# Optimization experiments

Measured on AMD Instinct MI355X. Metric: run time of the kernel, lower is better.

Reference implementation:

```python
import jax, jax.numpy as jnp
import numpy as np

B, N, A = 4096, 16, 8          # envs, num_agents, num_actions
D_IN, H1, DP, DZ = 128, 64, 64, 64  # obs dim, gnn hidden, obs_proc dim, gat fc dim


def _init(k, shape):
    return jax.random.normal(k, shape, jnp.float32) / np.sqrt(shape[0]).astype(np.float32)


def setup_inputs() -> dict:
    key = jax.random.key(0)
    ks = jax.random.split(key, 8)
    return {
        "obs": jax.random.normal(ks[0], (B * N, D_IN), jnp.float32),
        "policies": jax.random.uniform(ks[1], (B * N, A), dtype=jnp.float32),
        "actions": jax.random.uniform(ks[2], (B * N, A), dtype=jnp.float32),
        "W1": _init(ks[3], (D_IN, H1)), "b1": jnp.zeros((H1,), jnp.float32),
        "W2": _init(ks[4], (H1, DP)), "b2": jnp.zeros((DP,), jnp.float32),
        "Wfc": _init(ks[5], (DP, DZ)),
        "Wattn": _init(ks[6], (2 * DZ, 1)),
        "Wv": _init(ks[7], (DP + A, 1)), "bv": jnp.zeros((1,), jnp.float32),
    }


def reference(obs, policies, actions, W1, b1, W2, b2, Wfc, Wattn, Wv, bv):
    obs = obs.reshape(B, N, D_IN)
    # --- CriticInputPreprocess: two mean-aggregation GNN layers on a complete
    # graph with self-loops -> every node sees the per-env mean.
    agg1 = jnp.mean(obs, axis=1)                      # [B, D_IN]
    h = jax.nn.relu(agg1 @ W1 + b1)                   # [B, H1] (identical across nodes)
    obs_proc1 = h @ W2 + b2                           # mean of identical features is itself
    obs_proc = jnp.broadcast_to(obs_proc1[:, None, :], (B, N, DP))  # [B, N, DP]
    # --- GATLayer edge attention: e_{d<-s} = leaky_relu(attn([z_s, z_d]))
    z_ = obs_proc @ Wfc                               # [B, N, DZ]
    a_src = (z_ @ Wattn[:DZ]).squeeze(-1)             # [B, N]
    a_dst = (z_ @ Wattn[DZ:]).squeeze(-1)             # [B, N]
    e = jax.nn.leaky_relu(a_src[:, None, :] + a_dst[:, :, None])    # [B, dst, src]
    w = jax.nn.sigmoid(e)                             # [B, N, N]
    pi = policies.reshape(B, N, A)
    act = actions.reshape(B, N, A)
    # mailbox mix per (dst d, src k): z = w*act_k + (1-w)*pi_k
    z = w[..., None] * act[:, None, :, :] + (1.0 - w[..., None]) * pi[:, None, :, :]  # [B,d,k,A]
    # place_policies/place_zs + mean over src axis collapses to:
    # y[b,d,j] = (pi[b,j] + sum_{k!=j} z[b,d,k]) / N
    y = (jnp.sum(z, axis=2, keepdims=True) - z + pi[:, None, :, :]) / N               # [B,d,j,A]
    obs_rep = jnp.broadcast_to(obs_proc[:, None, :, :], (B, N, N, DP))                # obs_proc[b, j]
    obs_final = jnp.concatenate([obs_rep, y], axis=-1).reshape(B * N, N, DP + A)
    x = obs_final @ Wv + bv                           # [B*N, N, 1]
    return x, w.reshape(B * N, N, 1)
```

## Files before the change

kernel.cpp:

```cpp
#include <hip/hip_runtime.h>

#define BB   4096
#define NN   16
#define AA   8
#define DIN  128
#define H1C  64
#define DPC  64
#define DZC  64

#define GENV 8
#define WENV 4
#define NTHR 128

__global__ __launch_bounds__(NTHR, 1)
void critic_kernel(const float* __restrict__ obs,
                   const float* __restrict__ policies,
                   const float* __restrict__ actions,
                   const float* __restrict__ W1,
                   const float* __restrict__ b1,
                   const float* __restrict__ W2,
                   const float* __restrict__ b2,
                   const float* __restrict__ Wfc,
                   const float* __restrict__ Wattn,
                   const float* __restrict__ Wv,
                   const float* __restrict__ bv,
                   float* __restrict__ out_x,
                   float* __restrict__ out_w)
{
    __shared__ float sW1[DIN * H1C];
    __shared__ float sW2[H1C * DPC];
    __shared__ float sWfc[DPC * DZC];
    __shared__ float sAgg[GENV][DIN];
    __shared__ float sH[GENV][H1C];
    __shared__ float sP[GENV][DPC];
    __shared__ float sDv[GENV][16];

    const int tid = threadIdx.x;
    const int l   = tid & 63;
    const int wv  = tid >> 6;
    const int le0 = wv * WENV;
    const int e0  = blockIdx.x * GENV + le0;

    const float b1v = b1[l];
    const float b2v = b2[l];
    const float wa0 = Wattn[l];
    const float wa1 = Wattn[DZC + l];
    const float wvv = Wv[l];
    const float va  = Wv[64 + (l & 7)];
    const float bvv = bv[0];

    {
        const float4* g1 = reinterpret_cast<const float4*>(W1);
        float4*       s1 = reinterpret_cast<float4*>(sW1);
        #pragma unroll
        for (int i = 0; i < (DIN * H1C / 4) / NTHR; ++i)
            s1[i * NTHR + tid] = g1[i * NTHR + tid];
        const float4* g2 = reinterpret_cast<const float4*>(W2);
        float4*       s2 = reinterpret_cast<float4*>(sW2);
        #pragma unroll
        for (int i = 0; i < (H1C * DPC / 4) / NTHR; ++i)
            s2[i * NTHR + tid] = g2[i * NTHR + tid];
        const float4* g3 = reinterpret_cast<const float4*>(Wfc);
        float4*       s3 = reinterpret_cast<float4*>(sWfc);
        #pragma unroll
        for (int i = 0; i < (DPC * DZC / 4) / NTHR; ++i)
            s3[i * NTHR + tid] = g3[i * NTHR + tid];
    }

    #pragma unroll
    for (int ee = 0; ee < WENV; ++ee) {
        const float4* o4 = reinterpret_cast<const float4*>(obs + (size_t)(e0 + ee) * NN * DIN);
        float4 a = make_float4(0.f, 0.f, 0.f, 0.f);
        #pragma unroll
        for (int t = 0; t < 8; ++t) {
            const float4 v = o4[t * 64 + l];
            a.x += v.x; a.y += v.y; a.z += v.z; a.w += v.w;
        }
        a.x += __shfl_xor(a.x, 32);
        a.y += __shfl_xor(a.y, 32);
        a.z += __shfl_xor(a.z, 32);
        a.w += __shfl_xor(a.w, 32);
        if (l < 32) {
            const float inv = 1.0f / 16.0f;
            reinterpret_cast<float4*>(sAgg[le0 + ee])[l] =
                make_float4(a.x * inv, a.y * inv, a.z * inv, a.w * inv);
        }
    }

    float pv0[WENV], pv1[WENV], av0[WENV], av1[WENV];
    #pragma unroll
    for (int ee = 0; ee < WENV; ++ee) {
        const float* Pb = policies + (size_t)(e0 + ee) * (NN * AA);
        const float* Ab = actions  + (size_t)(e0 + ee) * (NN * AA);
        pv0[ee] = Pb[l]; pv1[ee] = Pb[64 + l];
        av0[ee] = Ab[l]; av1[ee] = Ab[64 + l];
    }

    __syncthreads();

    float acc0 = b1v, acc1 = b1v, acc2 = b1v, acc3 = b1v;
    #pragma unroll 8
    for (int d4 = 0; d4 < DIN / 4; ++d4) {
        const float w0  = sW1[(4 * d4 + 0) * H1C + l];
        const float w1_ = sW1[(4 * d4 + 1) * H1C + l];
        const float w2_ = sW1[(4 * d4 + 2) * H1C + l];
        const float w3_ = sW1[(4 * d4 + 3) * H1C + l];
        const float4 a0 = *reinterpret_cast<const float4*>(&sAgg[le0 + 0][4 * d4]);
        const float4 a1 = *reinterpret_cast<const float4*>(&sAgg[le0 + 1][4 * d4]);
        const float4 a2 = *reinterpret_cast<const float4*>(&sAgg[le0 + 2][4 * d4]);
        const float4 a3 = *reinterpret_cast<const float4*>(&sAgg[le0 + 3][4 * d4]);
        acc0 = fmaf(a0.x, w0, acc0); acc0 = fmaf(a0.y, w1_, acc0);
        acc0 = fmaf(a0.z, w2_, acc0); acc0 = fmaf(a0.w, w3_, acc0);
        acc1 = fmaf(a1.x, w0, acc1); acc1 = fmaf(a1.y, w1_, acc1);
        acc1 = fmaf(a1.z, w2_, acc1); acc1 = fmaf(a1.w, w3_, acc1);
        acc2 = fmaf(a2.x, w0, acc2); acc2 = fmaf(a2.y, w1_, acc2);
        acc2 = fmaf(a2.z, w2_, acc2); acc2 = fmaf(a2.w, w3_, acc2);
        acc3 = fmaf(a3.x, w0, acc3); acc3 = fmaf(a3.y, w1_, acc3);
        acc3 = fmaf(a3.z, w2_, acc3); acc3 = fmaf(a3.w, w3_, acc3);
    }
    sH[le0 + 0][l] = fmaxf(acc0, 0.0f);
    sH[le0 + 1][l] = fmaxf(acc1, 0.0f);
    sH[le0 + 2][l] = fmaxf(acc2, 0.0f);
    sH[le0 + 3][l] = fmaxf(acc3, 0.0f);

    __syncthreads();

    acc0 = b2v; acc1 = b2v; acc2 = b2v; acc3 = b2v;
    #pragma unroll
    for (int k4 = 0; k4 < H1C / 4; ++k4) {
        const float w0  = sW2[(4 * k4 + 0) * DPC + l];
        const float w1_ = sW2[(4 * k4 + 1) * DPC + l];
        const float w2_ = sW2[(4 * k4 + 2) * DPC + l];
        const float w3_ = sW2[(4 * k4 + 3) * DPC + l];
        const float4 a0 = *reinterpret_cast<const float4*>(&sH[le0 + 0][4 * k4]);
        const float4 a1 = *reinterpret_cast<const float4*>(&sH[le0 + 1][4 * k4]);
        const float4 a2 = *reinterpret_cast<const float4*>(&sH[le0 + 2][4 * k4]);
        const float4 a3 = *reinterpret_cast<const float4*>(&sH[le0 + 3][4 * k4]);
        acc0 = fmaf(a0.x, w0, acc0); acc0 = fmaf(a0.y, w1_, acc0);
        acc0 = fmaf(a0.z, w2_, acc0); acc0 = fmaf(a0.w, w3_, acc0);
        acc1 = fmaf(a1.x, w0, acc1); acc1 = fmaf(a1.y, w1_, acc1);
        acc1 = fmaf(a1.z, w2_, acc1); acc1 = fmaf(a1.w, w3_, acc1);
        acc2 = fmaf(a2.x, w0, acc2); acc2 = fmaf(a2.y, w1_, acc2);
        acc2 = fmaf(a2.z, w2_, acc2); acc2 = fmaf(a2.w, w3_, acc2);
        acc3 = fmaf(a3.x, w0, acc3); acc3 = fmaf(a3.y, w1_, acc3);
        acc3 = fmaf(a3.z, w2_, acc3); acc3 = fmaf(a3.w, w3_, acc3);
    }
    sP[le0 + 0][l] = acc0;
    sP[le0 + 1][l] = acc1;
    sP[le0 + 2][l] = acc2;
    sP[le0 + 3][l] = acc3;

    __syncthreads();

    float z0 = 0.f, z1 = 0.f, z2 = 0.f, z3 = 0.f;
    #pragma unroll
    for (int k4 = 0; k4 < DPC / 4; ++k4) {
        const float w0  = sWfc[(4 * k4 + 0) * DZC + l];
        const float w1_ = sWfc[(4 * k4 + 1) * DZC + l];
        const float w2_ = sWfc[(4 * k4 + 2) * DZC + l];
        const float w3_ = sWfc[(4 * k4 + 3) * DZC + l];
        const float4 a0 = *reinterpret_cast<const float4*>(&sP[le0 + 0][4 * k4]);
        const float4 a1 = *reinterpret_cast<const float4*>(&sP[le0 + 1][4 * k4]);
        const float4 a2 = *reinterpret_cast<const float4*>(&sP[le0 + 2][4 * k4]);
        const float4 a3 = *reinterpret_cast<const float4*>(&sP[le0 + 3][4 * k4]);
        z0 = fmaf(a0.x, w0, z0); z0 = fmaf(a0.y, w1_, z0);
        z0 = fmaf(a0.z, w2_, z0); z0 = fmaf(a0.w, w3_, z0);
        z1 = fmaf(a1.x, w0, z1); z1 = fmaf(a1.y, w1_, z1);
        z1 = fmaf(a1.z, w2_, z1); z1 = fmaf(a1.w, w3_, z1);
        z2 = fmaf(a2.x, w0, z2); z2 = fmaf(a2.y, w1_, z2);
        z2 = fmaf(a2.z, w2_, z2); z2 = fmaf(a2.w, w3_, z2);
        z3 = fmaf(a3.x, w0, z3); z3 = fmaf(a3.y, w1_, z3);
        z3 = fmaf(a3.z, w2_, z3); z3 = fmaf(a3.w, w3_, z3);
    }
    const float zz[WENV] = {z0, z1, z2, z3};

    float wgt[WENV], cc[WENV], Svv[WENV];
    #pragma unroll
    for (int ee = 0; ee < WENV; ++ee) {
        const int le = le0 + ee;
        float t0 = zz[ee] * (wa0 + wa1);
        float t1 = sP[le][l] * wvv;
        #pragma unroll
        for (int m = 32; m >= 1; m >>= 1) {
            t0 += __shfl_xor(t0, m);
            t1 += __shfl_xor(t1, m);
        }
        const float eV = (t0 > 0.0f) ? t0 : 0.01f * t0;
        wgt[ee] = 1.0f / (1.0f + expf(-eV));
        cc[ee]  = t1 + bvv;

        float q0 = (pv0[ee] - av0[ee]) * va;
        float q1 = (pv1[ee] - av1[ee]) * va;
        float fq = q0 + q1;
        float fp = (pv0[ee] + pv1[ee]) * va;
        #pragma unroll
        for (int m = 1; m <= 4; m <<= 1) {
            q0 += __shfl_xor(q0, m);
            q1 += __shfl_xor(q1, m);
        }
        #pragma unroll
        for (int m = 32; m >= 1; m >>= 1) {
            fq += __shfl_xor(fq, m);
            fp += __shfl_xor(fp, m);
        }
        Svv[ee] = fp - wgt[ee] * fq;

        if ((l & 7) == 0) {
            sDv[le][l >> 3]       = q0;
            sDv[le][8 + (l >> 3)] = q1;
        }
    }

    __syncthreads();

    const float invN = 1.0f / 16.0f;
    const int j0 = (4 * l) & 15;
    #pragma unroll
    for (int ee = 0; ee < WENV; ++ee) {
        const int le = le0 + ee;
        float4 xo, wo;
        xo.x = fmaf(wgt[ee], sDv[le][j0 + 0], Svv[ee]) * invN + cc[ee];
        xo.y = fmaf(wgt[ee], sDv[le][j0 + 1], Svv[ee]) * invN + cc[ee];
        xo.z = fmaf(wgt[ee], sDv[le][j0 + 2], Svv[ee]) * invN + cc[ee];
        xo.w = fmaf(wgt[ee], sDv[le][j0 + 3], Svv[ee]) * invN + cc[ee];
        wo.x = wo.y = wo.z = wo.w = wgt[ee];

        const size_t base = (size_t)(e0 + ee) * (NN * NN) + 4 * l;
        *reinterpret_cast<float4*>(out_x + base) = xo;
        *reinterpret_cast<float4*>(out_w + base) = wo;
    }
}

extern "C" void kernel_launch(void* const* d_in, const int* in_sizes, int n_in,
                              void* d_out, int out_size, void* d_ws, size_t ws_size,
                              hipStream_t stream) {
    const float* obs      = (const float*)d_in[0];
    const float* policies = (const float*)d_in[1];
    const float* actions  = (const float*)d_in[2];
    const float* W1       = (const float*)d_in[3];
    const float* b1       = (const float*)d_in[4];
    const float* W2       = (const float*)d_in[5];
    const float* b2       = (const float*)d_in[6];
    const float* Wfc      = (const float*)d_in[7];
    const float* Wattn    = (const float*)d_in[8];
    const float* Wv       = (const float*)d_in[9];
    const float* bv       = (const float*)d_in[10];

    float* out_x = (float*)d_out;
    float* out_w = out_x + (size_t)BB * NN * NN;

    critic_kernel<<<BB / GENV, NTHR, 0, stream>>>(obs, policies, actions,
                                                  W1, b1, W2, b2, Wfc, Wattn, Wv, bv,
                                                  out_x, out_w);
}
```

Measured before the change: 21.00 us.

## Fold W2, Wfc and attention/value weights into per-block vectors

Uses associativity to collapse the W2 and Wfc matmuls into two 64-vectors: u = Wfc·(wa_src+wa_dst) and v1 = W2·u, v2 = W2·Wv, plus bias scalars. After the W1 layer, each env then needs only dot products instead of two more 64x64 matmuls and their shared-memory staging and barriers. It also changes block shape to 256 threads with 2 envs per wave and allows two blocks per CU. The trade-off is that every block recomputes the folded vectors from global W2/Wfc, and the rounding order changes slightly.

```diff
diff --git a/kernel.cpp b/kernel.cpp
--- a/kernel.cpp
+++ b/kernel.cpp
@@ -9,10 +9,10 @@
 #define DZC  64
 
 #define GENV 8
-#define WENV 4
-#define NTHR 128
-
-__global__ __launch_bounds__(NTHR, 1)
+#define WENV 2
+#define NTHR 256
+
+__global__ __launch_bounds__(NTHR, 2)
 void critic_kernel(const float* __restrict__ obs,
                    const float* __restrict__ policies,
                    const float* __restrict__ actions,
@@ -28,11 +28,10 @@
                    float* __restrict__ out_w)
 {
     __shared__ float sW1[DIN * H1C];
-    __shared__ float sW2[H1C * DPC];
-    __shared__ float sWfc[DPC * DZC];
     __shared__ float sAgg[GENV][DIN];
-    __shared__ float sH[GENV][H1C];
-    __shared__ float sP[GENV][DPC];
+    __shared__ float sWsum[DZC];
+    __shared__ float sWv64[DPC];
+    __shared__ float sU[DPC];
     __shared__ float sDv[GENV][16];
 
     const int tid = threadIdx.x;
@@ -55,16 +54,6 @@
         #pragma unroll
         for (int i = 0; i < (DIN * H1C / 4) / NTHR; ++i)
             s1[i * NTHR + tid] = g1[i * NTHR + tid];
-        const float4* g2 = reinterpret_cast<const float4*>(W2);
-        float4*       s2 = reinterpret_cast<float4*>(sW2);
-        #pragma unroll
-        for (int i = 0; i < (H1C * DPC / 4) / NTHR; ++i)
-            s2[i * NTHR + tid] = g2[i * NTHR + tid];
-        const float4* g3 = reinterpret_cast<const float4*>(Wfc);
-        float4*       s3 = reinterpret_cast<float4*>(sWfc);
-        #pragma unroll
-        for (int i = 0; i < (DPC * DZC / 4) / NTHR; ++i)
-            s3[i * NTHR + tid] = g3[i * NTHR + tid];
     }
 
     #pragma unroll
@@ -96,9 +85,54 @@
         av0[ee] = Ab[l]; av1[ee] = Ab[64 + l];
     }
 
+    if (tid < 64) {
+        sWsum[l] = wa0 + wa1;
+        sWv64[l] = wvv;
+    }
+
     __syncthreads();
 
-    float acc0 = b1v, acc1 = b1v, acc2 = b1v, acc3 = b1v;
+    float u = 0.0f;
+    {
+        const float4* WfcR = reinterpret_cast<const float4*>(Wfc + (size_t)l * DZC);
+        const float4* ws4  = reinterpret_cast<const float4*>(sWsum);
+        #pragma unroll
+        for (int j4 = 0; j4 < DZC / 4; ++j4) {
+            const float4 w = WfcR[j4];
+            const float4 s = ws4[j4];
+            u = fmaf(w.x, s.x, u); u = fmaf(w.y, s.y, u);
+            u = fmaf(w.z, s.z, u); u = fmaf(w.w, s.w, u);
+        }
+    }
+    sU[l] = u;
+
+    __syncthreads();
+
+    float v1 = 0.0f, v2 = 0.0f;
+    {
+        const float4* W2R = reinterpret_cast<const float4*>(W2 + (size_t)l * DPC);
+        const float4* su4 = reinterpret_cast<const float4*>(sU);
+        const float4* sv4 = reinterpret_cast<const float4*>(sWv64);
+        #pragma unroll
+        for (int j4 = 0; j4 < DPC / 4; ++j4) {
+            const float4 w = W2R[j4];
+            const float4 a = su4[j4];
+            const float4 b = sv4[j4];
+            v1 = fmaf(w.x, a.x, v1); v1 = fmaf(w.y, a.y, v1);
+            v1 = fmaf(w.z, a.z, v1); v1 = fmaf(w.w, a.w, v1);
+            v2 = fmaf(w.x, b.x, v2); v2 = fmaf(w.y, b.y, v2);
+            v2 = fmaf(w.z, b.z, v2); v2 = fmaf(w.w, b.w, v2);
+        }
+    }
+    float tb2u = b2v * u;
+    float tb2w = b2v * wvv;
+    #pragma unroll
+    for (int m = 32; m >= 1; m >>= 1) {
+        tb2u += __shfl_xor(tb2u, m);
+        tb2w += __shfl_xor(tb2w, m);
+    }
+
+    float acc0 = b1v, acc1 = b1v;
     #pragma unroll 8
     for (int d4 = 0; d4 < DIN / 4; ++d4) {
         const float w0  = sW1[(4 * d4 + 0) * H1C + l];
@@ -107,87 +141,28 @@
         const float w3_ = sW1[(4 * d4 + 3) * H1C + l];
         const float4 a0 = *reinterpret_cast<const float4*>(&sAgg[le0 + 0][4 * d4]);
         const float4 a1 = *reinterpret_cast<const float4*>(&sAgg[le0 + 1][4 * d4]);
-        const float4 a2 = *reinterpret_cast<const float4*>(&sAgg[le0 + 2][4 * d4]);
-        const float4 a3 = *reinterpret_cast<const float4*>(&sAgg[le0 + 3][4 * d4]);
         acc0 = fmaf(a0.x, w0, acc0); acc0 = fmaf(a0.y, w1_, acc0);
         acc0 = fmaf(a0.z, w2_, acc0); acc0 = fmaf(a0.w, w3_, acc0);
         acc1 = fmaf(a1.x, w0, acc1); acc1 = fmaf(a1.y, w1_, acc1);
         acc1 = fmaf(a1.z, w2_, acc1); acc1 = fmaf(a1.w, w3_, acc1);
-        acc2 = fmaf(a2.x, w0, acc2); acc2 = fmaf(a2.y, w1_, acc2);
-        acc2 = fmaf(a2.z, w2_, acc2); acc2 = fmaf(a2.w, w3_, acc2);
-        acc3 = fmaf(a3.x, w0, acc3); acc3 = fmaf(a3.y, w1_, acc3);
-        acc3 = fmaf(a3.z, w2_, acc3); acc3 = fmaf(a3.w, w3_, acc3);
-    }
-    sH[le0 + 0][l] = fmaxf(acc0, 0.0f);
-    sH[le0 + 1][l] = fmaxf(acc1, 0.0f);
-    sH[le0 + 2][l] = fmaxf(acc2, 0.0f);
-    sH[le0 + 3][l] = fmaxf(acc3, 0.0f);
-
-    __syncthreads();
-
-    acc0 = b2v; acc1 = b2v; acc2 = b2v; acc3 = b2v;
-    #pragma unroll
-    for (int k4 = 0; k4 < H1C / 4; ++k4) {
-        const float w0  = sW2[(4 * k4 + 0) * DPC + l];
-        const float w1_ = sW2[(4 * k4 + 1) * DPC + l];
-        const float w2_ = sW2[(4 * k4 + 2) * DPC + l];
-        const float w3_ = sW2[(4 * k4 + 3) * DPC + l];
-        const float4 a0 = *reinterpret_cast<const float4*>(&sH[le0 + 0][4 * k4]);
-        const float4 a1 = *reinterpret_cast<const float4*>(&sH[le0 + 1][4 * k4]);
-        const float4 a2 = *reinterpret_cast<const float4*>(&sH[le0 + 2][4 * k4]);
-        const float4 a3 = *reinterpret_cast<const float4*>(&sH[le0 + 3][4 * k4]);
-        acc0 = fmaf(a0.x, w0, acc0); acc0 = fmaf(a0.y, w1_, acc0);
-        acc0 = fmaf(a0.z, w2_, acc0); acc0 = fmaf(a0.w, w3_, acc0);
-        acc1 = fmaf(a1.x, w0, acc1); acc1 = fmaf(a1.y, w1_, acc1);
-        acc1 = fmaf(a1.z, w2_, acc1); acc1 = fmaf(a1.w, w3_, acc1);
-        acc2 = fmaf(a2.x, w0, acc2); acc2 = fmaf(a2.y, w1_, acc2);
-        acc2 = fmaf(a2.z, w2_, acc2); acc2 = fmaf(a2.w, w3_, acc2);
-        acc3 = fmaf(a3.x, w0, acc3); acc3 = fmaf(a3.y, w1_, acc3);
-        acc3 = fmaf(a3.z, w2_, acc3); acc3 = fmaf(a3.w, w3_, acc3);
-    }
-    sP[le0 + 0][l] = acc0;
-    sP[le0 + 1][l] = acc1;
-    sP[le0 + 2][l] = acc2;
-    sP[le0 + 3][l] = acc3;
-
-    __syncthreads();
-
-    float z0 = 0.f, z1 = 0.f, z2 = 0.f, z3 = 0.f;
-    #pragma unroll
-    for (int k4 = 0; k4 < DPC / 4; ++k4) {
-        const float w0  = sWfc[(4 * k4 + 0) * DZC + l];
-        const float w1_ = sWfc[(4 * k4 + 1) * DZC + l];
-        const float w2_ = sWfc[(4 * k4 + 2) * DZC + l];
-        const float w3_ = sWfc[(4 * k4 + 3) * DZC + l];
-        const float4 a0 = *reinterpret_cast<const float4*>(&sP[le0 + 0][4 * k4]);
-        const float4 a1 = *reinterpret_cast<const float4*>(&sP[le0 + 1][4 * k4]);
-        const float4 a2 = *reinterpret_cast<const float4*>(&sP[le0 + 2][4 * k4]);
-        const float4 a3 = *reinterpret_cast<const float4*>(&sP[le0 + 3][4 * k4]);
-        z0 = fmaf(a0.x, w0, z0); z0 = fmaf(a0.y, w1_, z0);
-        z0 = fmaf(a0.z, w2_, z0); z0 = fmaf(a0.w, w3_, z0);
-        z1 = fmaf(a1.x, w0, z1); z1 = fmaf(a1.y, w1_, z1);
-        z1 = fmaf(a1.z, w2_, z1); z1 = fmaf(a1.w, w3_, z1);
-        z2 = fmaf(a2.x, w0, z2); z2 = fmaf(a2.y, w1_, z2);
-        z2 = fmaf(a2.z, w2_, z2); z2 = fmaf(a2.w, w3_, z2);
-        z3 = fmaf(a3.x, w0, z3); z3 = fmaf(a3.y, w1_, z3);
-        z3 = fmaf(a3.z, w2_, z3); z3 = fmaf(a3.w, w3_, z3);
-    }
-    const float zz[WENV] = {z0, z1, z2, z3};
+    }
+    const float hh[WENV] = { fmaxf(acc0, 0.0f), fmaxf(acc1, 0.0f) };
 
     float wgt[WENV], cc[WENV], Svv[WENV];
     #pragma unroll
     for (int ee = 0; ee < WENV; ++ee) {
         const int le = le0 + ee;
-        float t0 = zz[ee] * (wa0 + wa1);
-        float t1 = sP[le][l] * wvv;
+        float t0 = hh[ee] * v1;
+        float t1 = hh[ee] * v2;
         #pragma unroll
         for (int m = 32; m >= 1; m >>= 1) {
             t0 += __shfl_xor(t0, m);
             t1 += __shfl_xor(t1, m);
         }
-        const float eV = (t0 > 0.0f) ? t0 : 0.01f * t0;
+        const float logit = t0 + tb2u;
+        const float eV = (logit > 0.0f) ? logit : 0.01f * logit;
         wgt[ee] = 1.0f / (1.0f + expf(-eV));
-        cc[ee]  = t1 + bvv;
+        cc[ee]  = t1 + tb2w + bvv;
 
         float q0 = (pv0[ee] - av0[ee]) * va;
         float q1 = (pv1[ee] - av1[ee]) * va;
```

Measured after the change: 24.23 us. 1.15x slower.
